# Optimization experiments

Measured on AMD Instinct MI355X. Metric: run time of the kernel, lower is better.

The kernel has to match this reference:

```python
import jax, jax.numpy as jnp
import numpy as np

EPS = 1e-4
LN_EPS = 1e-5  # torch LayerNorm default
N, E, IN_DIM, OUT_DIM = 100000, 800000, 128, 128


def setup_inputs() -> dict:
    key = jax.random.key(0)
    ks = jax.random.split(key, 8)
    s = 1.0 / np.sqrt(IN_DIM)
    return {
        "x": jax.random.normal(ks[0], (N, IN_DIM), dtype=jnp.float32),
        "edge_index": jax.random.randint(ks[1], (2, E), 0, N, dtype=jnp.int32),
        "degree": jax.random.randint(ks[2], (N,), 0, 16, dtype=jnp.int32),
        "W_fc": jax.random.normal(ks[3], (IN_DIM, OUT_DIM), dtype=jnp.float32) * s,
        "b_fc": jax.random.normal(ks[4], (OUT_DIM,), dtype=jnp.float32) * s,
        "W_rate": jax.random.normal(ks[5], (IN_DIM, OUT_DIM), dtype=jnp.float32) * s,
        "W_rob": jax.random.normal(ks[6], (IN_DIM, OUT_DIM), dtype=jnp.float32) * s,
        "b_rob": jax.random.normal(ks[7], (OUT_DIM,), dtype=jnp.float32) * s,
        "ln_gamma": jnp.ones((OUT_DIM,), dtype=jnp.float32),
        "ln_beta": jnp.zeros((OUT_DIM,), dtype=jnp.float32),
    }


def reference(x, edge_index, degree, W_fc, b_fc, W_rate, W_rob, b_rob, ln_gamma, ln_beta):
    n = x.shape[0]
    rate = jax.nn.softplus(x @ W_rate) + EPS            # [N, D_out]
    gamma = x @ W_rob + b_rob                           # [N, D_out]
    h = x @ W_fc + b_fc                                 # [N, D_out]
    row, col = edge_index[0], edge_index[1]
    msg = h[row] + h[col]                               # [E, D_out] gather-add
    agg = jax.ops.segment_sum(msg, row, num_segments=n) # scatter_sum over dst
    deg = degree.astype(x.dtype)[:, None]
    y = (rate * agg + gamma) / (1.0 + rate * deg + EPS)
    mean = jnp.mean(y, axis=-1, keepdims=True)
    var = jnp.var(y, axis=-1, keepdims=True)
    y = (y - mean) * jax.lax.rsqrt(var + LN_EPS) * ln_gamma + ln_beta
    return y  # act is Identity
```

## Files before the change

### kernel.cpp

```cpp
#include <hip/hip_runtime.h>
#include <hip/hip_bf16.h>
#include <math.h>

#define NN 100000
#define DIM 128
#define EPSF 1e-4f
#define LN_EPSF 1e-5f
#define XSTR 136
#define NTILES 3125
#define TPB 4
#define GEMM_GRID ((NTILES + TPB - 1) / TPB)
#define CAP 32

typedef float  floatx4 __attribute__((ext_vector_type(4)));
typedef short  shortx8 __attribute__((ext_vector_type(8)));

__device__ __forceinline__ ushort f2b(float f) {
    union { float f; unsigned u; } c; c.f = f;
    unsigned lsb = (c.u >> 16) & 1u;
    return (ushort)((c.u + 0x7fffu + lsb) >> 16);
}
__device__ __forceinline__ float b2f(ushort b) {
    union { unsigned u; float f; } c; c.u = ((unsigned)b) << 16;
    return c.f;
}
__device__ __forceinline__ unsigned pk2(float a, float b) {
    union { __hip_bfloat162 h2; unsigned u; } c;
    c.h2 = __float22bfloat162_rn(float2{a, b});
    return c.u;
}

__global__ __launch_bounds__(256) void gemm3_mfma_kernel(
    const float* __restrict__ x,
    const float* __restrict__ Wfc, const float* __restrict__ Wrate,
    const float* __restrict__ Wrob,
    const float* __restrict__ bfc, const float* __restrict__ brob,
    ushort* __restrict__ h, ushort* __restrict__ rate, ushort* __restrict__ gam,
    const int* __restrict__ ei, int* __restrict__ cur,
    int* __restrict__ bucket, int E)
{
    __shared__ ushort xs[32 * XSTR];
    __shared__ ushort outb[3 * 32 * XSTR];
    const int tid  = threadIdx.x;
    const int wv   = tid >> 6;
    const int lane = tid & 63;

    for (int e = blockIdx.x * 256 + tid; e < E; e += GEMM_GRID * 256) {
        const int row = ei[e];
        const int col = ei[E + e];
        const int pos = atomicAdd(&cur[row], 1);
        if (pos < CAP) bucket[(size_t)row * CAP + pos] = col;
    }

    const float* Ws[3] = {Wfc, Wrate, Wrob};
    shortx8 bfrag[3][2][4];
#pragma unroll
    for (int w = 0; w < 3; ++w)
#pragma unroll
        for (int t = 0; t < 2; ++t) {
            const int n = (wv * 2 + t) * 16 + (lane & 15);
#pragma unroll
            for (int ks = 0; ks < 4; ++ks) {
                const int kb = ks * 32 + (lane >> 4) * 8;
                union { shortx8 v; ushort u[8]; } tmp;
#pragma unroll
                for (int j = 0; j < 8; ++j)
                    tmp.u[j] = f2b(Ws[w][(size_t)(kb + j) * DIM + n]);
                bfrag[w][t][ks] = tmp.v;
            }
        }

    float4 bias_fc[2], bias_rob[2];
#pragma unroll
    for (int t = 0; t < 2; ++t) {
        const int colbase = wv * 32 + t * 16 + (lane >> 4) * 4;
        bias_fc[t]  = ((const float4*)bfc)[colbase >> 2];
        bias_rob[t] = ((const float4*)brob)[colbase >> 2];
    }

    const int tile0  = blockIdx.x * TPB;
    const int ntiles = (NTILES - tile0 < TPB) ? (NTILES - tile0) : TPB;

    {
        const size_t row0 = (size_t)tile0 * 32;
#pragma unroll
        for (int k = 0; k < 4; ++k) {
            const int i = tid + k * 256, r = i >> 5, c4 = i & 31;
            const float4 v = ((const float4*)(x + (row0 + r) * DIM))[c4];
            uint2 uu; uu.x = pk2(v.x, v.y); uu.y = pk2(v.z, v.w);
            *(uint2*)&xs[r * XSTR + c4 * 4] = uu;
        }
    }
    __syncthreads();

    for (int ti = 0; ti < ntiles; ++ti) {
        const size_t row0 = (size_t)(tile0 + ti) * 32;
        const bool hasnext = (ti + 1 < ntiles);

        float4 pf[4];
        if (hasnext) {
            const size_t nrow0 = row0 + 32;
#pragma unroll
            for (int k = 0; k < 4; ++k) {
                const int i = tid + k * 256, r = i >> 5, c4 = i & 31;
                pf[k] = ((const float4*)(x + (nrow0 + r) * DIM))[c4];
            }
        }

#pragma unroll
        for (int rt = 0; rt < 2; ++rt) {
            shortx8 af[4];
#pragma unroll
            for (int ks = 0; ks < 4; ++ks)
                af[ks] = *(const shortx8*)&xs[(rt * 16 + (lane & 15)) * XSTR
                                              + ks * 32 + (lane >> 4) * 8];
            floatx4 acc[3][2] = {};
#pragma unroll
            for (int ks = 0; ks < 4; ++ks)
#pragma unroll
                for (int w = 0; w < 3; ++w)
#pragma unroll
                    for (int t = 0; t < 2; ++t)
                        acc[w][t] = __builtin_amdgcn_mfma_f32_16x16x32_bf16(
                            bfrag[w][t][ks], af[ks], acc[w][t], 0, 0, 0);

            const int node = rt * 16 + (lane & 15);
#pragma unroll
            for (int t = 0; t < 2; ++t) {
                const int colbase = wv * 32 + t * 16 + (lane >> 4) * 4;
                {
                    uint2 st;
                    st.x = pk2(acc[0][t][0] + bias_fc[t].x, acc[0][t][1] + bias_fc[t].y);
                    st.y = pk2(acc[0][t][2] + bias_fc[t].z, acc[0][t][3] + bias_fc[t].w);
                    *(uint2*)&outb[0 * 32 * XSTR + node * XSTR + colbase] = st;
                }
                {
                    float rv[4];
#pragma unroll
                    for (int r = 0; r < 4; ++r) {
                        const float v = acc[1][t][r];
                        rv[r] = fmaxf(v, 0.f) + __logf(1.f + __expf(-fabsf(v))) + EPSF;
                    }
                    uint2 st; st.x = pk2(rv[0], rv[1]); st.y = pk2(rv[2], rv[3]);
                    *(uint2*)&outb[1 * 32 * XSTR + node * XSTR + colbase] = st;
                }
                {
                    uint2 st;
                    st.x = pk2(acc[2][t][0] + bias_rob[t].x, acc[2][t][1] + bias_rob[t].y);
                    st.y = pk2(acc[2][t][2] + bias_rob[t].z, acc[2][t][3] + bias_rob[t].w);
                    *(uint2*)&outb[2 * 32 * XSTR + node * XSTR + colbase] = st;
                }
            }
        }
        __syncthreads();

#pragma unroll
        for (int k = 0; k < 6; ++k) {
            const int w = k >> 1;
            const int rem = tid + (k & 1) * 256;
            const int node = rem >> 4, seg = rem & 15;
            const uint4 v = *(const uint4*)&outb[w * 32 * XSTR + node * XSTR + seg * 8];
            ushort* dstw = (w == 0) ? h : (w == 1) ? rate : gam;
            *(uint4*)(dstw + (row0 + node) * DIM + seg * 8) = v;
        }

        if (hasnext) {
#pragma unroll
            for (int k = 0; k < 4; ++k) {
                const int i = tid + k * 256, r = i >> 5, c4 = i & 31;
                uint2 uu; uu.x = pk2(pf[k].x, pf[k].y); uu.y = pk2(pf[k].z, pf[k].w);
                *(uint2*)&xs[r * XSTR + c4 * 4] = uu;
            }
        }
        __syncthreads();
    }
}

__global__ __launch_bounds__(256) void finalize_kernel(
    const ushort* __restrict__ h, const ushort* __restrict__ rate,
    const ushort* __restrict__ gam,
    const int* __restrict__ cur, const int* __restrict__ bucket,
    const int* __restrict__ degree,
    const float* __restrict__ ln_g, const float* __restrict__ ln_b,
    float* __restrict__ out)
{
    const int wave = threadIdx.x >> 6;
    const int lane = threadIdx.x & 63;
    const size_t r0 = (size_t)blockIdx.x * 16 + wave * 4;
    const unsigned* hu = (const unsigned*)h;

    int nR[4]; float dgR[4]; int bvR[4];
    unsigned hvR[4], rvR[4], gvR[4];
#pragma unroll
    for (int q = 0; q < 4; ++q) {
        const size_t r = r0 + q;
        nR[q]  = cur[r];
        dgR[q] = (float)degree[r];
        bvR[q] = bucket[r * CAP + (lane & 31)];
        hvR[q] = hu[r * 64 + lane];
        rvR[q] = ((const unsigned*)rate)[r * 64 + lane];
        gvR[q] = ((const unsigned*)gam)[r * 64 + lane];
    }
    const float2 lg = ((const float2*)ln_g)[lane];
    const float2 lb = ((const float2*)ln_b)[lane];

    float ax[4] = {0.f, 0.f, 0.f, 0.f}, ay[4] = {0.f, 0.f, 0.f, 0.f};
    const int mx = max(max(nR[0], nR[1]), max(nR[2], nR[3]));

    for (int j = 0; j < mx; j += 4) {
        unsigned v[4][4];
#pragma unroll
        for (int q = 0; q < 4; ++q)
#pragma unroll
            for (int p = 0; p < 4; ++p) {
                const int c = (j + p < nR[q]) ? __shfl(bvR[q], j + p, 64) : 0;
                v[q][p] = hu[(size_t)c * 64 + lane];
            }
#pragma unroll
        for (int q = 0; q < 4; ++q)
#pragma unroll
            for (int p = 0; p < 4; ++p) {
                const bool ok = (j + p < nR[q]);
                ax[q] += ok ? b2f((ushort)(v[q][p] & 0xffff)) : 0.f;
                ay[q] += ok ? b2f((ushort)(v[q][p] >> 16))    : 0.f;
            }
    }

#pragma unroll
    for (int q = 0; q < 4; ++q) {
        const size_t row = r0 + q;
        const float cn = (float)nR[q];
        const float dg = dgR[q];

        const float h0 = b2f((ushort)(hvR[q] & 0xffff)), h1 = b2f((ushort)(hvR[q] >> 16));
        const float r0f = b2f((ushort)(rvR[q] & 0xffff)), r1f = b2f((ushort)(rvR[q] >> 16));
        const float g0 = b2f((ushort)(gvR[q] & 0xffff)), g1 = b2f((ushort)(gvR[q] >> 16));

        const float a0 = cn * h0 + ax[q];
        const float a1 = cn * h1 + ay[q];
        const float y0 = (r0f * a0 + g0) / (1.f + r0f * dg + EPSF);
        const float y1 = (r1f * a1 + g1) / (1.f + r1f * dg + EPSF);

        float s  = y0 + y1;
        float s2 = y0 * y0 + y1 * y1;
#pragma unroll
        for (int o = 32; o > 0; o >>= 1) {
            s  += __shfl_xor(s,  o, 64);
            s2 += __shfl_xor(s2, o, 64);
        }
        const float mean = s * (1.f / 128.f);
        const float var  = s2 * (1.f / 128.f) - mean * mean;
        const float inv  = rsqrtf(var + LN_EPSF);

        float2 o;
        o.x = (y0 - mean) * inv * lg.x + lb.x;
        o.y = (y1 - mean) * inv * lg.y + lb.y;
        ((float2*)(out + row * DIM))[lane] = o;
    }
}

extern "C" void kernel_launch(void* const* d_in, const int* in_sizes, int n_in,
                              void* d_out, int out_size, void* d_ws, size_t ws_size,
                              hipStream_t stream)
{
    const float* x      = (const float*)d_in[0];
    const int*   ei     = (const int*)  d_in[1];
    const int*   degree = (const int*)  d_in[2];
    const float* Wfc    = (const float*)d_in[3];
    const float* bfc    = (const float*)d_in[4];
    const float* Wrate  = (const float*)d_in[5];
    const float* Wrob   = (const float*)d_in[6];
    const float* brob   = (const float*)d_in[7];
    const float* ln_g   = (const float*)d_in[8];
    const float* ln_b   = (const float*)d_in[9];
    float* out = (float*)d_out;

    const int E = in_sizes[1] / 2;
    const size_t NEL = (size_t)NN * DIM;

    ushort* h     = (ushort*)d_ws;
    ushort* rate  = h + NEL;
    ushort* gam   = rate + NEL;
    int*   cur    = (int*)(gam + NEL);
    int*   bucket = cur + NN;

    hipMemsetAsync(cur, 0, NN * sizeof(int), stream);
    gemm3_mfma_kernel<<<GEMM_GRID, 256, 0, stream>>>(x, Wfc, Wrate, Wrob,
                                                     bfc, brob, h, rate, gam,
                                                     ei, cur, bucket, E);
    finalize_kernel<<<NN / 16, 256, 0, stream>>>(h, rate, gam, cur, bucket,
                                                 degree, ln_g, ln_b, out);
}
```

Before: 239.7 us.

## Prepack bf16 weight fragments in a separate kernel and halve tiles per block

Adds a pack kernel that converts the three weight matrices to bf16 once, already laid out in MFMA fragment order, and zeroes the bucket counters in the same launch in place of the memset. The GEMM blocks then load their B fragments with vector loads instead of each block doing strided fp32 loads and conversions. Tiles per block drop from 4 to 2, doubling the grid, and each block now handles exactly 512 edges for bucketing instead of a grid-stride loop. This adds one extra kernel launch but removes redundant per-block weight conversion and spreads the work over more blocks.

```diff
diff --git a/kernel.cpp b/kernel.cpp
--- a/kernel.cpp
+++ b/kernel.cpp
@@ -8,8 +8,9 @@
 #define LN_EPSF 1e-5f
 #define XSTR 136
 #define NTILES 3125
-#define TPB 4
+#define TPB 2
 #define GEMM_GRID ((NTILES + TPB - 1) / TPB)
+#define PACK_GRID ((NN + 255) / 256)
 #define CAP 32
 
 typedef float  floatx4 __attribute__((ext_vector_type(4)));
@@ -30,10 +31,32 @@
     return c.u;
 }
 
+__global__ __launch_bounds__(256) void pack_kernel(
+    const float* __restrict__ Wfc, const float* __restrict__ Wrate,
+    const float* __restrict__ Wrob, ushort* __restrict__ Bpack,
+    int* __restrict__ cur)
+{
+    const int id = blockIdx.x * 256 + threadIdx.x;
+    if (id < NN) cur[id] = 0;
+    if (id >= 6144) return;
+    const int lane = id & 63;
+    const int ks   = (id >> 6) & 3;
+    const int nt   = (id >> 8) & 7;
+    const int w    = id >> 11;
+    const float* W = (w == 0) ? Wfc : (w == 1) ? Wrate : Wrob;
+    const int n  = nt * 16 + (lane & 15);
+    const int kb = ks * 32 + (lane >> 4) * 8;
+    ushort tmp[8];
+#pragma unroll
+    for (int j = 0; j < 8; ++j) tmp[j] = f2b(W[(kb + j) * DIM + n]);
+    ushort* dst = Bpack + (size_t)id * 8;
+#pragma unroll
+    for (int j = 0; j < 8; ++j) dst[j] = tmp[j];
+}
+
 __global__ __launch_bounds__(256) void gemm3_mfma_kernel(
     const float* __restrict__ x,
-    const float* __restrict__ Wfc, const float* __restrict__ Wrate,
-    const float* __restrict__ Wrob,
+    const ushort* __restrict__ Bpack,
     const float* __restrict__ bfc, const float* __restrict__ brob,
     ushort* __restrict__ h, ushort* __restrict__ rate, ushort* __restrict__ gam,
     const int* __restrict__ ei, int* __restrict__ cur,
@@ -45,28 +68,30 @@
     const int wv   = tid >> 6;
     const int lane = tid & 63;
 
-    for (int e = blockIdx.x * 256 + tid; e < E; e += GEMM_GRID * 256) {
-        const int row = ei[e];
-        const int col = ei[E + e];
-        const int pos = atomicAdd(&cur[row], 1);
-        if (pos < CAP) bucket[(size_t)row * CAP + pos] = col;
-    }
-
-    const float* Ws[3] = {Wfc, Wrate, Wrob};
+    {
+        const int e = blockIdx.x * 512 + tid;
+#pragma unroll
+        for (int q = 0; q < 2; ++q) {
+            const int ee = e + q * 256;
+            if (ee < E) {
+                const int row = ei[ee];
+                const int col = ei[E + ee];
+                const int pos = atomicAdd(&cur[row], 1);
+                if (pos < CAP) bucket[(size_t)row * CAP + pos] = col;
+            }
+        }
+    }
+
     shortx8 bfrag[3][2][4];
 #pragma unroll
     for (int w = 0; w < 3; ++w)
 #pragma unroll
         for (int t = 0; t < 2; ++t) {
-            const int n = (wv * 2 + t) * 16 + (lane & 15);
+            const int nt = wv * 2 + t;
 #pragma unroll
             for (int ks = 0; ks < 4; ++ks) {
-                const int kb = ks * 32 + (lane >> 4) * 8;
-                union { shortx8 v; ushort u[8]; } tmp;
-#pragma unroll
-                for (int j = 0; j < 8; ++j)
-                    tmp.u[j] = f2b(Ws[w][(size_t)(kb + j) * DIM + n]);
-                bfrag[w][t][ks] = tmp.v;
+                const ushort* p = Bpack + ((((size_t)w * 8 + nt) * 4 + ks) * 64 + lane) * 8;
+                bfrag[w][t][ks] = *(const shortx8*)p;
             }
         }
 
@@ -281,12 +306,13 @@
     ushort* h     = (ushort*)d_ws;
     ushort* rate  = h + NEL;
     ushort* gam   = rate + NEL;
-    int*   cur    = (int*)(gam + NEL);
+    ushort* Bpack = gam + NEL;
+    int*   cur    = (int*)(Bpack + 49152);
     int*   bucket = cur + NN;
 
-    hipMemsetAsync(cur, 0, NN * sizeof(int), stream);
-    gemm3_mfma_kernel<<<GEMM_GRID, 256, 0, stream>>>(x, Wfc, Wrate, Wrob,
-                                                     bfc, brob, h, rate, gam,
+    pack_kernel<<<PACK_GRID, 256, 0, stream>>>(Wfc, Wrate, Wrob, Bpack, cur);
+    gemm3_mfma_kernel<<<GEMM_GRID, 256, 0, stream>>>(x, Bpack, bfc, brob,
+                                                     h, rate, gam,
                                                      ei, cur, bucket, E);
     finalize_kernel<<<NN / 16, 256, 0, stream>>>(h, rate, gam, cur, bucket,
                                                  degree, ln_g, ln_b, out);
```

Result: faster. 218.0 us (-9.0%).
